# Optimization experiments

Measured on AMD Instinct MI355X. Metric: run time of the kernel, lower is better.

The kernel has to match this reference:

```python
import jax, jax.numpy as jnp
import numpy as np

N, E = 50000, 800000
IN_DIM, HID, HEADS, OUT_DIM = 7, 64, 4, 32
EPS = 1e-5


def gat_layer(x, src, dst, W, a_s, a_d, b, heads, ch, concat):
    # x: [N, F_in]; W: [F_in, heads*ch]; a_s,a_d: [heads, ch]; b: [heads*ch] or [ch]
    n = x.shape[0]
    h = (x @ W).reshape(n, heads, ch)
    e_src = jnp.sum(h * a_s, axis=-1)  # [N, heads]
    e_dst = jnp.sum(h * a_d, axis=-1)
    e = jax.nn.leaky_relu(e_src[src] + e_dst[dst], 0.2)  # [E, heads]
    m = jax.ops.segment_max(e, dst, num_segments=n)
    ex = jnp.exp(e - m[dst])
    denom = jax.ops.segment_sum(ex, dst, num_segments=n)
    alpha = ex / (denom[dst] + 1e-16)  # [E, heads]
    msg = h[src] * alpha[:, :, None]  # [E, heads, ch]
    out = jax.ops.segment_sum(msg, dst, num_segments=n)  # [N, heads, ch]
    out = out.reshape(n, heads * ch) if concat else out.mean(axis=1)
    return out + b


def batch_norm(x, g, be):
    mu = x.mean(axis=0)
    var = x.var(axis=0)
    return (x - mu) * jax.lax.rsqrt(var + EPS) * g + be


def setup_inputs() -> dict:
    key = jax.random.key(0)
    ks = jax.random.split(key, 24)
    d = {}
    d['x'] = jax.random.normal(ks[0], (N, IN_DIM), dtype=jnp.float32)
    d['edge_index'] = jax.random.randint(ks[1], (2, E), 0, N, dtype=jnp.int32)
    d['source_node'] = 123
    s = 0.1
    HC = HEADS * HID  # 256
    d['W1'] = jax.random.normal(ks[2], (IN_DIM, HC)) * s
    d['as1'] = jax.random.normal(ks[3], (HEADS, HID)) * s
    d['ad1'] = jax.random.normal(ks[4], (HEADS, HID)) * s
    d['b1'] = jnp.zeros((HC,))
    d['g1'] = jnp.ones((HC,))
    d['be1'] = jnp.zeros((HC,))
    d['W2'] = jax.random.normal(ks[5], (HC, HC)) * s
    d['as2'] = jax.random.normal(ks[6], (HEADS, HID)) * s
    d['ad2'] = jax.random.normal(ks[7], (HEADS, HID)) * s
    d['b2'] = jnp.zeros((HC,))
    d['g2'] = jnp.ones((HC,))
    d['be2'] = jnp.zeros((HC,))
    d['W3'] = jax.random.normal(ks[8], (HC, OUT_DIM)) * s
    d['as3'] = jax.random.normal(ks[9], (1, OUT_DIM)) * s
    d['ad3'] = jax.random.normal(ks[10], (1, OUT_DIM)) * s
    d['b3'] = jnp.zeros((OUT_DIM,))
    d['Wm1'] = jax.random.normal(ks[11], (2 * OUT_DIM, 64)) * s
    d['bm1'] = jnp.zeros((64,))
    d['Wm2'] = jax.random.normal(ks[12], (64, 32)) * s
    d['bm2'] = jnp.zeros((32,))
    d['Wm3'] = jax.random.normal(ks[13], (32, 1)) * s
    d['bm3'] = jnp.zeros((1,))
    return d


def reference(x, edge_index, source_node, W1, as1, ad1, b1, g1, be1,
              W2, as2, ad2, b2, g2, be2, W3, as3, ad3, b3,
              Wm1, bm1, Wm2, bm2, Wm3, bm3):
    n = x.shape[0]
    loop = jnp.arange(n, dtype=edge_index.dtype)
    src = jnp.concatenate([edge_index[0], loop])  # PyG GATConv adds self-loops
    dst = jnp.concatenate([edge_index[1], loop])
    h = gat_layer(x, src, dst, W1, as1, ad1, b1, HEADS, HID, True)
    h = jax.nn.relu(batch_norm(h, g1, be1))
    h = gat_layer(h, src, dst, W2, as2, ad2, b2, HEADS, HID, True)
    h = jax.nn.relu(batch_norm(h, g2, be2))
    emb = gat_layer(h, src, dst, W3, as3, ad3, b3, 1, OUT_DIM, False)  # [N, 32]
    src_emb = jnp.broadcast_to(emb[source_node][None, :], (n, OUT_DIM))
    z = jnp.concatenate([src_emb, emb], axis=1)  # [N, 64]
    z = jax.nn.relu(z @ Wm1 + bm1)
    z = jax.nn.relu(z @ Wm2 + bm2)
    scores = jax.nn.sigmoid(z @ Wm3 + bm3)
    return scores.squeeze(-1)
```

## Files before the change

kernel.cpp:

```cpp
#include <hip/hip_runtime.h>
#include <hip/hip_fp16.h>
#include <math.h>

#define NN 50000
#define EE 800000
#define ETOT (EE + NN)
#define HC 256
#define HEADS 4
#define OUTD 32
#define NB1 196

typedef _Float16 f16x8 __attribute__((ext_vector_type(8)));
typedef float f32x4 __attribute__((ext_vector_type(4)));

__device__ __forceinline__ float wred_sum(float v) {
#pragma unroll
  for (int off = 32; off; off >>= 1) v += __shfl_xor(v, off);
  return v;
}
__device__ __forceinline__ float lrelu(float x) { return x >= 0.f ? x : 0.2f * x; }

__global__ void zero_i32(int* __restrict__ p, int n) {
  int i = blockIdx.x * blockDim.x + threadIdx.x;
  if (i < n) p[i] = 0;
}

__global__ void hist_k(const int* __restrict__ ei, int* __restrict__ cnt) {
  int e = blockIdx.x * blockDim.x + threadIdx.x;
  if (e >= ETOT) return;
  int d = (e < EE) ? ei[EE + e] : (e - EE);
  atomicAdd(&cnt[d], 1);
}

__global__ void scan1_k(const int* __restrict__ cnt, int* __restrict__ part,
                        int* __restrict__ bsum) {
  __shared__ int s[256];
  int t = threadIdx.x, i = blockIdx.x * 256 + t;
  int v = (i < NN) ? cnt[i] : 0;
  s[t] = v;
  __syncthreads();
#pragma unroll
  for (int off = 1; off < 256; off <<= 1) {
    int u = (t >= off) ? s[t - off] : 0;
    __syncthreads();
    s[t] += u;
    __syncthreads();
  }
  if (i < NN) part[i] = s[t] - v;
  if (t == 255) bsum[blockIdx.x] = s[255];
}

__global__ void scan2_k(const int* __restrict__ bsum, int* __restrict__ bscan) {
  __shared__ int s[256];
  int t = threadIdx.x;
  int v = (t < NB1) ? bsum[t] : 0;
  s[t] = v;
  __syncthreads();
#pragma unroll
  for (int off = 1; off < 256; off <<= 1) {
    int u = (t >= off) ? s[t - off] : 0;
    __syncthreads();
    s[t] += u;
    __syncthreads();
  }
  if (t < NB1) bscan[t] = s[t] - v;
}

__global__ void scan3_k(const int* __restrict__ part, const int* __restrict__ bscan,
                        int* __restrict__ offs, int* __restrict__ cursor) {
  int i = blockIdx.x * 256 + threadIdx.x;
  if (i < NN) {
    int v = part[i] + bscan[blockIdx.x];
    offs[i] = v;
    cursor[i] = v;
  }
  if (i == 0) offs[NN] = ETOT;
}

__global__ void scatter_k(const int* __restrict__ ei, int* __restrict__ cursor,
                          int* __restrict__ elist) {
  int e = blockIdx.x * blockDim.x + threadIdx.x;
  if (e >= ETOT) return;
  int s, d;
  if (e < EE) { s = ei[e]; d = ei[EE + e]; } else { s = d = e - EE; }
  int pos = atomicAdd(&cursor[d], 1);
  elist[pos] = s;
}

template <int NCOL>
__global__ __launch_bounds__(256) void wswz_k(const float* __restrict__ W,
                                              __half* __restrict__ Bh) {
  int idx = blockIdx.x * 256 + threadIdx.x;
  if (idx >= HC * NCOL) return;
  int k = idx / NCOL, n = idx % NCOL;
  int frag = (n >> 4) * 8 + (k >> 5);
  int lane = (n & 15) + (((k >> 3) & 3) << 4);
  int elem = k & 7;
  Bh[(frag * 64 + lane) * 8 + elem] = __float2half(W[idx]);
}

__global__ __launch_bounds__(256) void l1_h_k(
    const float* __restrict__ x, const float* __restrict__ W1,
    const float* __restrict__ asf, const float* __restrict__ adf,
    __half* __restrict__ hb, float* __restrict__ es, float* __restrict__ ed) {
  int t = threadIdx.x, w = t >> 6;
  float wc[7];
#pragma unroll
  for (int k = 0; k < 7; ++k) wc[k] = W1[k * HC + t];
  float av = asf[t], dv = adf[t];
  for (int i = blockIdx.x; i < NN; i += gridDim.x) {
    float acc = 0.f;
#pragma unroll
    for (int k = 0; k < 7; ++k) acc = fmaf(x[i * 7 + k], wc[k], acc);
    hb[(size_t)i * HC + t] = __float2half(acc);
    float a = wred_sum(acc * av);
    float d = wred_sum(acc * dv);
    if ((t & 63) == 0) { es[i * HEADS + w] = a; ed[i * HEADS + w] = d; }
  }
}

__global__ __launch_bounds__(256) void gat_agg256(
    const __half* __restrict__ hb, const float* __restrict__ es,
    const float* __restrict__ ed, const int* __restrict__ offs,
    const int* __restrict__ elist, const float* __restrict__ bias,
    float* __restrict__ out) {
  int t = threadIdx.x, wv = t >> 6, lane = t & 63;
  int hd = lane >> 4;
  float4 bv = ((const float4*)bias)[lane];
  const float2* hb4 = (const float2*)hb;
  int i = blockIdx.x * 4 + wv;
  if (i >= NN) return;
  int base = offs[i], end = offs[i + 1];
  float edv = ed[i * HEADS + hd];
  float denom = 0.f;
  float4 acc = make_float4(0.f, 0.f, 0.f, 0.f);

#define EDGE1(SRC)                                         \
  {                                                        \
    int src_ = (SRC);                                      \
    float ex_ = __expf(lrelu(es[src_ * HEADS + hd] + edv));\
    denom += ex_;                                          \
    float2 raw_ = hb4[(size_t)src_ * 64 + lane];           \
    float2 h01_ = __half22float2(*(__half2*)&raw_.x);      \
    float2 h23_ = __half22float2(*(__half2*)&raw_.y);      \
    acc.x = fmaf(ex_, h01_.x, acc.x);                      \
    acc.y = fmaf(ex_, h01_.y, acc.y);                      \
    acc.z = fmaf(ex_, h23_.x, acc.z);                      \
    acc.w = fmaf(ex_, h23_.y, acc.w);                      \
  }

  int e = base;
  int alim = (base + 3) & ~3;
  for (; e < end && e < alim; ++e) EDGE1(elist[e]);
  for (; e + 4 <= end; e += 4) {
    int4 idx = *(const int4*)&elist[e];
    float e0 = es[idx.x * HEADS + hd], e1 = es[idx.y * HEADS + hd];
    float e2 = es[idx.z * HEADS + hd], e3 = es[idx.w * HEADS + hd];
    float2 r0 = hb4[(size_t)idx.x * 64 + lane];
    float2 r1 = hb4[(size_t)idx.y * 64 + lane];
    float2 r2 = hb4[(size_t)idx.z * 64 + lane];
    float2 r3 = hb4[(size_t)idx.w * 64 + lane];
    float x0 = __expf(lrelu(e0 + edv)), x1 = __expf(lrelu(e1 + edv));
    float x2 = __expf(lrelu(e2 + edv)), x3 = __expf(lrelu(e3 + edv));
    denom += (x0 + x1) + (x2 + x3);
    float2 a0 = __half22float2(*(__half2*)&r0.x), b0 = __half22float2(*(__half2*)&r0.y);
    float2 a1 = __half22float2(*(__half2*)&r1.x), b1 = __half22float2(*(__half2*)&r1.y);
    float2 a2 = __half22float2(*(__half2*)&r2.x), b2 = __half22float2(*(__half2*)&r2.y);
    float2 a3 = __half22float2(*(__half2*)&r3.x), b3 = __half22float2(*(__half2*)&r3.y);
    acc.x = fmaf(x0, a0.x, fmaf(x1, a1.x, fmaf(x2, a2.x, fmaf(x3, a3.x, acc.x))));
    acc.y = fmaf(x0, a0.y, fmaf(x1, a1.y, fmaf(x2, a2.y, fmaf(x3, a3.y, acc.y))));
    acc.z = fmaf(x0, b0.x, fmaf(x1, b1.x, fmaf(x2, b2.x, fmaf(x3, b3.x, acc.z))));
    acc.w = fmaf(x0, b0.y, fmaf(x1, b1.y, fmaf(x2, b2.y, fmaf(x3, b3.y, acc.w))));
  }
  for (; e < end; ++e) EDGE1(elist[e]);
#undef EDGE1

  float inv = 1.f / (denom + 1e-16f);
  float4 r;
  r.x = fmaf(acc.x, inv, bv.x);
  r.y = fmaf(acc.y, inv, bv.y);
  r.z = fmaf(acc.z, inv, bv.z);
  r.w = fmaf(acc.w, inv, bv.w);
  ((float4*)(out + (size_t)i * HC))[lane] = r;
}

__global__ __launch_bounds__(256) void bn_stats_k(const float* __restrict__ X,
                                                  float* __restrict__ sums) {
  int t = threadIdx.x;
  int r0 = blockIdx.x * 64;
  int rend = min(r0 + 64, NN);
  float s = 0.f, q = 0.f;
  for (int r = r0; r < rend; ++r) {
    float v = X[(size_t)r * HC + t];
    s += v;
    q = fmaf(v, v, q);
  }
  atomicAdd(&sums[t], s);
  atomicAdd(&sums[HC + t], q);
}

__global__ void bn_final_k(const float* __restrict__ sums, const float* __restrict__ g,
                           const float* __restrict__ be, float* __restrict__ ab) {
  int t = threadIdx.x;
  float mu = sums[t] * (1.f / NN);
  float var = sums[HC + t] * (1.f / NN) - mu * mu;
  float a = g[t] * rsqrtf(var + 1e-5f);
  ab[t] = a;
  ab[HC + t] = fmaf(-mu, a, be[t]);
}

__global__ __launch_bounds__(256) void gemm_mfma_k(const float* __restrict__ A,
                                                   const __half* __restrict__ Bh,
                                                   const float* __restrict__ ab,
                                                   __half* __restrict__ Ch) {
  __shared__ __align__(16) __half As[128 * 40];
  __shared__ float abL[512];
  int t = threadIdx.x;
  abL[t] = ab[t];
  abL[256 + t] = ab[256 + t];
  int wv = t >> 6, lane = t & 63;
  int wm = wv >> 1, wn = wv & 1;
  int m0 = blockIdx.x * 128;
  int ntb = blockIdx.y * 8 + wn * 4;
  int srow = t >> 1;
  int skq = (t & 1) * 16;
  int grow = m0 + srow;
  const f16x8* Bf = (const f16x8*)Bh;

  f32x4 acc[4][4];
  f32x4 zf = {0.f, 0.f, 0.f, 0.f};
#pragma unroll
  for (int mt = 0; mt < 4; ++mt)
#pragma unroll
    for (int nt = 0; nt < 4; ++nt) acc[mt][nt] = zf;

  for (int ks = 0; ks < 8; ++ks) {
    int k0 = ks * 32;
    __syncthreads();
    {
      float xv[16];
      if (grow < NN) {
        const float* ap = A + (size_t)grow * HC + k0 + skq;
#pragma unroll
        for (int q = 0; q < 4; ++q) *(float4*)&xv[q * 4] = *(const float4*)(ap + q * 4);
      } else {
#pragma unroll
        for (int j = 0; j < 16; ++j) xv[j] = 0.f;
      }
      f16x8 v0, v1;
#pragma unroll
      for (int j = 0; j < 8; ++j) {
        float a_ = abL[k0 + skq + j], b_ = abL[256 + k0 + skq + j];
        v0[j] = (_Float16)fmaxf(fmaf(xv[j], a_, b_), 0.f);
      }
#pragma unroll
      for (int j = 0; j < 8; ++j) {
        float a_ = abL[k0 + skq + 8 + j], b_ = abL[256 + k0 + skq + 8 + j];
        v1[j] = (_Float16)fmaxf(fmaf(xv[8 + j], a_, b_), 0.f);
      }
      *(f16x8*)&As[srow * 40 + skq] = v0;
      *(f16x8*)&As[srow * 40 + skq + 8] = v1;
    }
    __syncthreads();
    f16x8 af[4], bf[4];
    int lr = wm * 64 + (lane & 15);
    int kk = (lane >> 4) * 8;
#pragma unroll
    for (int mt = 0; mt < 4; ++mt)
      af[mt] = *(const f16x8*)&As[(lr + mt * 16) * 40 + kk];
#pragma unroll
    for (int nt = 0; nt < 4; ++nt)
      bf[nt] = Bf[(size_t)((ntb + nt) * 8 + ks) * 64 + lane];
#pragma unroll
    for (int mt = 0; mt < 4; ++mt)
#pragma unroll
      for (int nt = 0; nt < 4; ++nt)
        acc[mt][nt] = __builtin_amdgcn_mfma_f32_16x16x32_f16(af[mt], bf[nt], acc[mt][nt], 0, 0, 0);
  }

  int colb = blockIdx.y * 128 + wn * 64 + (lane & 15);
#pragma unroll
  for (int mt = 0; mt < 4; ++mt) {
    int rowb = m0 + wm * 64 + mt * 16 + (lane >> 4) * 4;
#pragma unroll
    for (int nt = 0; nt < 4; ++nt) {
      int col = colb + nt * 16;
#pragma unroll
      for (int r = 0; r < 4; ++r) {
        int row = rowb + r;
        if (row < NN) Ch[(size_t)row * HC + col] = __float2half(acc[mt][nt][r]);
      }
    }
  }
}

__global__ __launch_bounds__(256) void l3_mfma_k(const float* __restrict__ A,
                                                 const __half* __restrict__ Bh,
                                                 const float* __restrict__ ab,
                                                 float* __restrict__ h3) {
  __shared__ __align__(16) __half As[128 * 40];
  __shared__ float abL[512];
  int t = threadIdx.x;
  abL[t] = ab[t];
  abL[256 + t] = ab[256 + t];
  int wv = t >> 6, lane = t & 63;
  int m0 = blockIdx.x * 128;
  int srow = t >> 1;
  int skq = (t & 1) * 16;
  int grow = m0 + srow;
  const f16x8* Bf = (const f16x8*)Bh;

  f32x4 acc[2][2];
  f32x4 zf = {0.f, 0.f, 0.f, 0.f};
#pragma unroll
  for (int mt = 0; mt < 2; ++mt)
#pragma unroll
    for (int nt = 0; nt < 2; ++nt) acc[mt][nt] = zf;

  for (int ks = 0; ks < 8; ++ks) {
    int k0 = ks * 32;
    __syncthreads();
    {
      float xv[16];
      if (grow < NN) {
        const float* ap = A + (size_t)grow * HC + k0 + skq;
#pragma unroll
        for (int q = 0; q < 4; ++q) *(float4*)&xv[q * 4] = *(const float4*)(ap + q * 4);
      } else {
#pragma unroll
        for (int j = 0; j < 16; ++j) xv[j] = 0.f;
      }
      f16x8 v0, v1;
#pragma unroll
      for (int j = 0; j < 8; ++j) {
        float a_ = abL[k0 + skq + j], b_ = abL[256 + k0 + skq + j];
        v0[j] = (_Float16)fmaxf(fmaf(xv[j], a_, b_), 0.f);
      }
#pragma unroll
      for (int j = 0; j < 8; ++j) {
        float a_ = abL[k0 + skq + 8 + j], b_ = abL[256 + k0 + skq + 8 + j];
        v1[j] = (_Float16)fmaxf(fmaf(xv[8 + j], a_, b_), 0.f);
      }
      *(f16x8*)&As[srow * 40 + skq] = v0;
      *(f16x8*)&As[srow * 40 + skq + 8] = v1;
    }
    __syncthreads();
    f16x8 af[2], bf[2];
    int lr = wv * 32 + (lane & 15);
    int kk = (lane >> 4) * 8;
#pragma unroll
    for (int mt = 0; mt < 2; ++mt)
      af[mt] = *(const f16x8*)&As[(lr + mt * 16) * 40 + kk];
#pragma unroll
    for (int nt = 0; nt < 2; ++nt)
      bf[nt] = Bf[(size_t)(nt * 8 + ks) * 64 + lane];
#pragma unroll
    for (int mt = 0; mt < 2; ++mt)
#pragma unroll
      for (int nt = 0; nt < 2; ++nt)
        acc[mt][nt] = __builtin_amdgcn_mfma_f32_16x16x32_f16(af[mt], bf[nt], acc[mt][nt], 0, 0, 0);
  }

#pragma unroll
  for (int mt = 0; mt < 2; ++mt) {
    int rowb = m0 + wv * 32 + mt * 16 + (lane >> 4) * 4;
#pragma unroll
    for (int nt = 0; nt < 2; ++nt) {
      int col = nt * 16 + (lane & 15);
#pragma unroll
      for (int r = 0; r < 4; ++r) {
        int row = rowb + r;
        if (row < NN) h3[(size_t)row * OUTD + col] = acc[mt][nt][r];
      }
    }
  }
}

__global__ __launch_bounds__(256) void esed3_k(const float* __restrict__ h3,
                                               const float* __restrict__ asf,
                                               const float* __restrict__ adf,
                                               float* __restrict__ es3,
                                               float* __restrict__ ed3) {
  int t = threadIdx.x;
  int node = blockIdx.x * 8 + (t >> 5);
  int c = t & 31;
  if (node >= NN) return;
  float v = h3[(size_t)node * OUTD + c];
  float a = v * asf[c], d = v * adf[c];
#pragma unroll
  for (int off = 16; off; off >>= 1) {
    a += __shfl_xor(a, off);
    d += __shfl_xor(d, off);
  }
  if (c == 0) { es3[node] = a; ed3[node] = d; }
}

__global__ __launch_bounds__(256) void esed_k(const __half* __restrict__ hb,
                                              const float* __restrict__ asf,
                                              const float* __restrict__ adf,
                                              float* __restrict__ es,
                                              float* __restrict__ ed) {
  int t = threadIdx.x, w = t >> 6;
  float av = asf[t], dv = adf[t];
  for (int i = blockIdx.x; i < NN; i += gridDim.x) {
    float v = __half2float(hb[(size_t)i * HC + t]);
    float a = wred_sum(v * av);
    float d = wred_sum(v * dv);
    if ((t & 63) == 0) { es[i * HEADS + w] = a; ed[i * HEADS + w] = d; }
  }
}

__global__ __launch_bounds__(256) void gat_agg32(
    const float* __restrict__ h3, const float* __restrict__ es3,
    const float* __restrict__ ed3, const int* __restrict__ offs,
    const int* __restrict__ elist, const float* __restrict__ b3,
    float* __restrict__ emb) {
  int t = threadIdx.x, wv = t >> 6, lane = t & 63;
  int eo = lane >> 5, c = lane & 31;
  float bv = b3[c];
  int i = blockIdx.x * 4 + wv;
  if (i >= NN) return;
  int base = offs[i], end = offs[i + 1];
  float edv = ed3[i];
  float denom = 0.f, acc = 0.f;
#pragma unroll 2
  for (int e = base + eo; e < end; e += 2) {
    int src = elist[e];
    float ex = __expf(lrelu(es3[src] + edv));
    denom += ex;
    acc = fmaf(ex, h3[(size_t)src * OUTD + c], acc);
  }
  denom += __shfl_xor(denom, 32);
  acc += __shfl_xor(acc, 32);
  if (eo == 0) emb[(size_t)i * OUTD + c] = acc / (denom + 1e-16f) + bv;
}

__global__ void c1_k(const float* __restrict__ emb, const int* __restrict__ srcn,
                     const float* __restrict__ Wm1, const float* __restrict__ bm1,
                     float* __restrict__ c1) {
  int l = threadIdx.x;
  int sn = srcn[0];
  float a = bm1[l];
  for (int k = 0; k < 32; ++k) a = fmaf(emb[(size_t)sn * OUTD + k], Wm1[k * 64 + l], a);
  c1[l] = a;
}

__global__ __launch_bounds__(256) void mlp_k(
    const float* __restrict__ emb, const float* __restrict__ c1,
    const float* __restrict__ Wm1, const float* __restrict__ Wm2,
    const float* __restrict__ bm2, const float* __restrict__ Wm3,
    const float* __restrict__ bm3, float* __restrict__ outp) {
  __shared__ float WL1s[32][64];
  __shared__ float WL2s[64][32];
  __shared__ float W3s[32];
  __shared__ float c1s[64];
  int t = threadIdx.x;
  for (int q = t; q < 2048; q += 256) WL1s[q >> 6][q & 63] = Wm1[(32 + (q >> 6)) * 64 + (q & 63)];
  for (int q = t; q < 2048; q += 256) WL2s[q >> 5][q & 31] = Wm2[q];
  if (t < 32) W3s[t] = Wm3[t];
  if (t < 64) c1s[t] = c1[t];
  __syncthreads();
  int wv = t >> 6, lane = t & 63;
  int p = lane >> 5, c = lane & 31;
  float bm2v = bm2[c];
  float bm3v = bm3[0];
  for (int node = blockIdx.x * 4 + wv; node < NN; node += gridDim.x * 4) {
    float zv = (lane < 32) ? emb[(size_t)node * OUTD + lane] : 0.f;
    float a1 = c1s[lane];
#pragma unroll
    for (int k = 0; k < 32; ++k) a1 = fmaf(__shfl(zv, k), WL1s[k][lane], a1);
    float u1 = fmaxf(a1, 0.f);
    float a2 = 0.f;
#pragma unroll
    for (int j = 0; j < 32; ++j) a2 = fmaf(__shfl(u1, p * 32 + j), WL2s[p * 32 + j][c], a2);
    a2 += __shfl_xor(a2, 32);
    float v = 0.f;
    if (lane < 32) {
      float u2 = fmaxf(a2 + bm2v, 0.f);
      v = u2 * W3s[c];
    }
    v = wred_sum(v);
    if (lane == 0) outp[node] = 1.f / (1.f + __expf(-(v + bm3v)));
  }
}

extern "C" void kernel_launch(void* const* d_in, const int* in_sizes, int n_in,
                              void* d_out, int out_size, void* d_ws, size_t ws_size,
                              hipStream_t stream) {
  const float* x   = (const float*)d_in[0];
  const int* eidx  = (const int*)d_in[1];
  const int* srcn  = (const int*)d_in[2];
  const float* W1  = (const float*)d_in[3];
  const float* as1 = (const float*)d_in[4];
  const float* ad1 = (const float*)d_in[5];
  const float* b1  = (const float*)d_in[6];
  const float* g1  = (const float*)d_in[7];
  const float* be1 = (const float*)d_in[8];
  const float* W2  = (const float*)d_in[9];
  const float* as2 = (const float*)d_in[10];
  const float* ad2 = (const float*)d_in[11];
  const float* b2  = (const float*)d_in[12];
  const float* g2  = (const float*)d_in[13];
  const float* be2 = (const float*)d_in[14];
  const float* W3  = (const float*)d_in[15];
  const float* as3 = (const float*)d_in[16];
  const float* ad3 = (const float*)d_in[17];
  const float* b3  = (const float*)d_in[18];
  const float* Wm1 = (const float*)d_in[19];
  const float* bm1 = (const float*)d_in[20];
  const float* Wm2 = (const float*)d_in[21];
  const float* bm2 = (const float*)d_in[22];
  const float* Wm3 = (const float*)d_in[23];
  const float* bm3 = (const float*)d_in[24];
  float* outp = (float*)d_out;

  float* fw = (float*)d_ws;
  float* bufB   = fw;  fw += (size_t)NN * HC;
  __half* hbuf  = (__half*)fw; fw += (size_t)NN * HC / 2;
  float* h3     = fw;  fw += (size_t)NN * OUTD;
  float* emb    = fw;  fw += (size_t)NN * OUTD;
  float* es     = fw;  fw += (size_t)NN * HEADS;
  float* ed     = fw;  fw += (size_t)NN * HEADS;
  float* es3    = fw;  fw += NN;
  float* ed3    = fw;  fw += NN;
  float* bnsums = fw;  fw += 2 * HC;
  float* bnab   = fw;  fw += 2 * HC;
  float* c1     = fw;  fw += 64;
  __half* Bh    = (__half*)fw; fw += (size_t)HC * HC / 2;
  __half* Bh3   = (__half*)fw; fw += (size_t)HC * OUTD / 2;
  int* iw = (int*)fw;
  int* offs   = iw;  iw += NN + 4;
  int* cursor = iw;  iw += NN;
  int* elist  = iw;  iw += ETOT;
  int* part   = iw;  iw += NN;
  int* bsum   = iw;  iw += 256;
  int* bscan  = iw;  iw += 256;

  const int TB = 256;
  const int gE = (ETOT + TB - 1) / TB;
  const int gN4 = (NN + 3) / 4;

  zero_i32<<<(NN + TB - 1) / TB, TB, 0, stream>>>(cursor, NN);
  hist_k<<<gE, TB, 0, stream>>>(eidx, cursor);
  scan1_k<<<NB1, TB, 0, stream>>>(cursor, part, bsum);
  scan2_k<<<1, TB, 0, stream>>>(bsum, bscan);
  scan3_k<<<NB1, TB, 0, stream>>>(part, bscan, offs, cursor);
  scatter_k<<<gE, TB, 0, stream>>>(eidx, cursor, elist);
  wswz_k<HC><<<HC * HC / TB, TB, 0, stream>>>(W2, Bh);
  wswz_k<OUTD><<<HC * OUTD / TB, TB, 0, stream>>>(W3, Bh3);

  l1_h_k<<<2048, TB, 0, stream>>>(x, W1, as1, ad1, hbuf, es, ed);
  gat_agg256<<<gN4, TB, 0, stream>>>(hbuf, es, ed, offs, elist, b1, bufB);
  zero_i32<<<2, TB, 0, stream>>>((int*)bnsums, 2 * HC);
  bn_stats_k<<<(NN + 63) / 64, TB, 0, stream>>>(bufB, bnsums);
  bn_final_k<<<1, TB, 0, stream>>>(bnsums, g1, be1, bnab);

  gemm_mfma_k<<<dim3((NN + 127) / 128, HC / 128), TB, 0, stream>>>(bufB, Bh, bnab, hbuf);
  esed_k<<<2048, TB, 0, stream>>>(hbuf, as2, ad2, es, ed);
  gat_agg256<<<gN4, TB, 0, stream>>>(hbuf, es, ed, offs, elist, b2, bufB);
  zero_i32<<<2, TB, 0, stream>>>((int*)bnsums, 2 * HC);
  bn_stats_k<<<(NN + 63) / 64, TB, 0, stream>>>(bufB, bnsums);
  bn_final_k<<<1, TB, 0, stream>>>(bnsums, g2, be2, bnab);

  l3_mfma_k<<<(NN + 127) / 128, TB, 0, stream>>>(bufB, Bh3, bnab, h3);
  esed3_k<<<(NN + 7) / 8, TB, 0, stream>>>(h3, as3, ad3, es3, ed3);
  gat_agg32<<<gN4, TB, 0, stream>>>(h3, es3, ed3, offs, elist, b3, emb);

  c1_k<<<1, 64, 0, stream>>>(emb, srcn, Wm1, bm1, c1);
  mlp_k<<<512, TB, 0, stream>>>(emb, c1, Wm1, Wm2, bm2, Wm3, bm3, outp);
}
```

Baseline: 514.0 us.

## Store aggregation outputs in fp16 and fuse attention scores into GEMM epilogues

```diff
diff --git a/kernel.cpp b/kernel.cpp
--- a/kernel.cpp
+++ b/kernel.cpp
@@ -16,6 +16,11 @@
 __device__ __forceinline__ float wred_sum(float v) {
 #pragma unroll
   for (int off = 32; off; off >>= 1) v += __shfl_xor(v, off);
+  return v;
+}
+__device__ __forceinline__ float qred16(float v) {
+#pragma unroll
+  for (int off = 1; off < 16; off <<= 1) v += __shfl_xor(v, off);
   return v;
 }
 __device__ __forceinline__ float lrelu(float x) { return x >= 0.f ? x : 0.2f * x; }
@@ -123,7 +128,7 @@
     const __half* __restrict__ hb, const float* __restrict__ es,
     const float* __restrict__ ed, const int* __restrict__ offs,
     const int* __restrict__ elist, const float* __restrict__ bias,
-    float* __restrict__ out) {
+    __half* __restrict__ out) {
   int t = threadIdx.x, wv = t >> 6, lane = t & 63;
   int hd = lane >> 4;
   float4 bv = ((const float4*)bias)[lane];
@@ -135,63 +140,84 @@
   float denom = 0.f;
   float4 acc = make_float4(0.f, 0.f, 0.f, 0.f);
 
-#define EDGE1(SRC)                                         \
-  {                                                        \
-    int src_ = (SRC);                                      \
-    float ex_ = __expf(lrelu(es[src_ * HEADS + hd] + edv));\
-    denom += ex_;                                          \
-    float2 raw_ = hb4[(size_t)src_ * 64 + lane];           \
-    float2 h01_ = __half22float2(*(__half2*)&raw_.x);      \
-    float2 h23_ = __half22float2(*(__half2*)&raw_.y);      \
-    acc.x = fmaf(ex_, h01_.x, acc.x);                      \
-    acc.y = fmaf(ex_, h01_.y, acc.y);                      \
-    acc.z = fmaf(ex_, h23_.x, acc.z);                      \
-    acc.w = fmaf(ex_, h23_.y, acc.w);                      \
+#define ACC1(X_, R_)                                   \
+  {                                                    \
+    float2 h01_ = __half22float2(*(__half2*)&R_.x);    \
+    float2 h23_ = __half22float2(*(__half2*)&R_.y);    \
+    acc.x = fmaf(X_, h01_.x, acc.x);                   \
+    acc.y = fmaf(X_, h01_.y, acc.y);                   \
+    acc.z = fmaf(X_, h23_.x, acc.z);                   \
+    acc.w = fmaf(X_, h23_.y, acc.w);                   \
+  }
+#define EDGE1(SRC)                                          \
+  {                                                         \
+    int src_ = (SRC);                                       \
+    float ex_ = __expf(lrelu(es[src_ * HEADS + hd] + edv)); \
+    denom += ex_;                                           \
+    float2 raw_ = hb4[(size_t)src_ * 64 + lane];            \
+    ACC1(ex_, raw_);                                        \
   }
 
   int e = base;
   int alim = (base + 3) & ~3;
   for (; e < end && e < alim; ++e) EDGE1(elist[e]);
+  for (; e + 8 <= end; e += 8) {
+    int4 ia = *(const int4*)&elist[e];
+    int4 ib = *(const int4*)&elist[e + 4];
+    float f0 = es[ia.x * HEADS + hd], f1 = es[ia.y * HEADS + hd];
+    float f2 = es[ia.z * HEADS + hd], f3 = es[ia.w * HEADS + hd];
+    float f4 = es[ib.x * HEADS + hd], f5 = es[ib.y * HEADS + hd];
+    float f6 = es[ib.z * HEADS + hd], f7 = es[ib.w * HEADS + hd];
+    float2 r0 = hb4[(size_t)ia.x * 64 + lane];
+    float2 r1 = hb4[(size_t)ia.y * 64 + lane];
+    float2 r2 = hb4[(size_t)ia.z * 64 + lane];
+    float2 r3 = hb4[(size_t)ia.w * 64 + lane];
+    float2 r4 = hb4[(size_t)ib.x * 64 + lane];
+    float2 r5 = hb4[(size_t)ib.y * 64 + lane];
+    float2 r6 = hb4[(size_t)ib.z * 64 + lane];
+    float2 r7 = hb4[(size_t)ib.w * 64 + lane];
+    float x0 = __expf(lrelu(f0 + edv)), x1 = __expf(lrelu(f1 + edv));
+    float x2 = __expf(lrelu(f2 + edv)), x3 = __expf(lrelu(f3 + edv));
+    float x4 = __expf(lrelu(f4 + edv)), x5 = __expf(lrelu(f5 + edv));
+    float x6 = __expf(lrelu(f6 + edv)), x7 = __expf(lrelu(f7 + edv));
+    denom += ((x0 + x1) + (x2 + x3)) + ((x4 + x5) + (x6 + x7));
+    ACC1(x0, r0); ACC1(x1, r1); ACC1(x2, r2); ACC1(x3, r3);
+    ACC1(x4, r4); ACC1(x5, r5); ACC1(x6, r6); ACC1(x7, r7);
+  }
   for (; e + 4 <= end; e += 4) {
-    int4 idx = *(const int4*)&elist[e];
-    float e0 = es[idx.x * HEADS + hd], e1 = es[idx.y * HEADS + hd];
-    float e2 = es[idx.z * HEADS + hd], e3 = es[idx.w * HEADS + hd];
-    float2 r0 = hb4[(size_t)idx.x * 64 + lane];
-    float2 r1 = hb4[(size_t)idx.y * 64 + lane];
-    float2 r2 = hb4[(size_t)idx.z * 64 + lane];
-    float2 r3 = hb4[(size_t)idx.w * 64 + lane];
-    float x0 = __expf(lrelu(e0 + edv)), x1 = __expf(lrelu(e1 + edv));
-    float x2 = __expf(lrelu(e2 + edv)), x3 = __expf(lrelu(e3 + edv));
+    int4 ia = *(const int4*)&elist[e];
+    float f0 = es[ia.x * HEADS + hd], f1 = es[ia.y * HEADS + hd];
+    float f2 = es[ia.z * HEADS + hd], f3 = es[ia.w * HEADS + hd];
+    float2 r0 = hb4[(size_t)ia.x * 64 + lane];
+    float2 r1 = hb4[(size_t)ia.y * 64 + lane];
+    float2 r2 = hb4[(size_t)ia.z * 64 + lane];
+    float2 r3 = hb4[(size_t)ia.w * 64 + lane];
+    float x0 = __expf(lrelu(f0 + edv)), x1 = __expf(lrelu(f1 + edv));
+    float x2 = __expf(lrelu(f2 + edv)), x3 = __expf(lrelu(f3 + edv));
     denom += (x0 + x1) + (x2 + x3);
-    float2 a0 = __half22float2(*(__half2*)&r0.x), b0 = __half22float2(*(__half2*)&r0.y);
-    float2 a1 = __half22float2(*(__half2*)&r1.x), b1 = __half22float2(*(__half2*)&r1.y);
-    float2 a2 = __half22float2(*(__half2*)&r2.x), b2 = __half22float2(*(__half2*)&r2.y);
-    float2 a3 = __half22float2(*(__half2*)&r3.x), b3 = __half22float2(*(__half2*)&r3.y);
-    acc.x = fmaf(x0, a0.x, fmaf(x1, a1.x, fmaf(x2, a2.x, fmaf(x3, a3.x, acc.x))));
-    acc.y = fmaf(x0, a0.y, fmaf(x1, a1.y, fmaf(x2, a2.y, fmaf(x3, a3.y, acc.y))));
-    acc.z = fmaf(x0, b0.x, fmaf(x1, b1.x, fmaf(x2, b2.x, fmaf(x3, b3.x, acc.z))));
-    acc.w = fmaf(x0, b0.y, fmaf(x1, b1.y, fmaf(x2, b2.y, fmaf(x3, b3.y, acc.w))));
+    ACC1(x0, r0); ACC1(x1, r1); ACC1(x2, r2); ACC1(x3, r3);
   }
   for (; e < end; ++e) EDGE1(elist[e]);
 #undef EDGE1
+#undef ACC1
 
   float inv = 1.f / (denom + 1e-16f);
-  float4 r;
-  r.x = fmaf(acc.x, inv, bv.x);
-  r.y = fmaf(acc.y, inv, bv.y);
-  r.z = fmaf(acc.z, inv, bv.z);
-  r.w = fmaf(acc.w, inv, bv.w);
-  ((float4*)(out + (size_t)i * HC))[lane] = r;
-}
-
-__global__ __launch_bounds__(256) void bn_stats_k(const float* __restrict__ X,
+  __half2 o01 = __floats2half2_rn(fmaf(acc.x, inv, bv.x), fmaf(acc.y, inv, bv.y));
+  __half2 o23 = __floats2half2_rn(fmaf(acc.z, inv, bv.z), fmaf(acc.w, inv, bv.w));
+  uint2 pk;
+  pk.x = *(unsigned int*)&o01;
+  pk.y = *(unsigned int*)&o23;
+  ((uint2*)(out + (size_t)i * HC))[lane] = pk;
+}
+
+__global__ __launch_bounds__(256) void bn_stats_k(const __half* __restrict__ X,
                                                   float* __restrict__ sums) {
   int t = threadIdx.x;
   int r0 = blockIdx.x * 64;
   int rend = min(r0 + 64, NN);
   float s = 0.f, q = 0.f;
   for (int r = r0; r < rend; ++r) {
-    float v = X[(size_t)r * HC + t];
+    float v = __half2float(X[(size_t)r * HC + t]);
     s += v;
     q = fmaf(v, v, q);
   }
@@ -209,10 +235,14 @@
   ab[HC + t] = fmaf(-mu, a, be[t]);
 }
 
-__global__ __launch_bounds__(256) void gemm_mfma_k(const float* __restrict__ A,
+__global__ __launch_bounds__(256) void gemm_mfma_k(const __half* __restrict__ A,
                                                    const __half* __restrict__ Bh,
                                                    const float* __restrict__ ab,
-                                                   __half* __restrict__ Ch) {
+                                                   const float* __restrict__ asf,
+                                                   const float* __restrict__ adf,
+                                                   __half* __restrict__ Ch,
+                                                   float* __restrict__ es,
+                                                   float* __restrict__ ed) {
   __shared__ __align__(16) __half As[128 * 40];
   __shared__ float abL[512];
   int t = threadIdx.x;
@@ -240,9 +270,16 @@
     {
       float xv[16];
       if (grow < NN) {
-        const float* ap = A + (size_t)grow * HC + k0 + skq;
-#pragma unroll
-        for (int q = 0; q < 4; ++q) *(float4*)&xv[q * 4] = *(const float4*)(ap + q * 4);
+        const __half* ap = A + (size_t)grow * HC + k0 + skq;
+        __half2 hp[8];
+        *(uint4*)&hp[0] = *(const uint4*)ap;
+        *(uint4*)&hp[4] = *(const uint4*)(ap + 8);
+#pragma unroll
+        for (int j = 0; j < 8; ++j) {
+          float2 f = __half22float2(hp[j]);
+          xv[2 * j] = f.x;
+          xv[2 * j + 1] = f.y;
+        }
       } else {
 #pragma unroll
         for (int j = 0; j < 16; ++j) xv[j] = 0.f;
@@ -292,12 +329,43 @@
       }
     }
   }
-}
-
-__global__ __launch_bounds__(256) void l3_mfma_k(const float* __restrict__ A,
+  float asv[4], adv[4];
+#pragma unroll
+  for (int nt = 0; nt < 4; ++nt) {
+    asv[nt] = asf[colb + nt * 16];
+    adv[nt] = adf[colb + nt * 16];
+  }
+  int head = (blockIdx.y << 1) | wn;
+#pragma unroll
+  for (int mt = 0; mt < 4; ++mt) {
+    int rowb = m0 + wm * 64 + mt * 16 + (lane >> 4) * 4;
+#pragma unroll
+    for (int r = 0; r < 4; ++r) {
+      float pe = 0.f, pd = 0.f;
+#pragma unroll
+      for (int nt = 0; nt < 4; ++nt) {
+        pe = fmaf(acc[mt][nt][r], asv[nt], pe);
+        pd = fmaf(acc[mt][nt][r], adv[nt], pd);
+      }
+      pe = qred16(pe);
+      pd = qred16(pd);
+      int row = rowb + r;
+      if ((lane & 15) == 0 && row < NN) {
+        es[row * HEADS + head] = pe;
+        ed[row * HEADS + head] = pd;
+      }
+    }
+  }
+}
+
+__global__ __launch_bounds__(256) void l3_mfma_k(const __half* __restrict__ A,
                                                  const __half* __restrict__ Bh,
                                                  const float* __restrict__ ab,
-                                                 float* __restrict__ h3) {
+                                                 const float* __restrict__ asf,
+                                                 const float* __restrict__ adf,
+                                                 __half* __restrict__ h3,
+                                                 float* __restrict__ es3,
+                                                 float* __restrict__ ed3) {
   __shared__ __align__(16) __half As[128 * 40];
   __shared__ float abL[512];
   int t = threadIdx.x;
@@ -323,9 +391,16 @@
     {
       float xv[16];
       if (grow < NN) {
-        const float* ap = A + (size_t)grow * HC + k0 + skq;
-#pragma unroll
-        for (int q = 0; q < 4; ++q) *(float4*)&xv[q * 4] = *(const float4*)(ap + q * 4);
+        const __half* ap = A + (size_t)grow * HC + k0 + skq;
+        __half2 hp[8];
+        *(uint4*)&hp[0] = *(const uint4*)ap;
+        *(uint4*)&hp[4] = *(const uint4*)(ap + 8);
+#pragma unroll
+        for (int j = 0; j < 8; ++j) {
+          float2 f = __half22float2(hp[j]);
+          xv[2 * j] = f.x;
+          xv[2 * j + 1] = f.y;
+        }
       } else {
 #pragma unroll
         for (int j = 0; j < 16; ++j) xv[j] = 0.f;
@@ -361,57 +436,38 @@
         acc[mt][nt] = __builtin_amdgcn_mfma_f32_16x16x32_f16(af[mt], bf[nt], acc[mt][nt], 0, 0, 0);
   }
 
+  float as3v[2], ad3v[2];
+#pragma unroll
+  for (int nt = 0; nt < 2; ++nt) {
+    as3v[nt] = asf[nt * 16 + (lane & 15)];
+    ad3v[nt] = adf[nt * 16 + (lane & 15)];
+  }
 #pragma unroll
   for (int mt = 0; mt < 2; ++mt) {
     int rowb = m0 + wv * 32 + mt * 16 + (lane >> 4) * 4;
 #pragma unroll
-    for (int nt = 0; nt < 2; ++nt) {
-      int col = nt * 16 + (lane & 15);
-#pragma unroll
-      for (int r = 0; r < 4; ++r) {
-        int row = rowb + r;
-        if (row < NN) h3[(size_t)row * OUTD + col] = acc[mt][nt][r];
+    for (int r = 0; r < 4; ++r) {
+      int row = rowb + r;
+      float pe = 0.f, pd = 0.f;
+#pragma unroll
+      for (int nt = 0; nt < 2; ++nt) {
+        int col = nt * 16 + (lane & 15);
+        if (row < NN) h3[(size_t)row * OUTD + col] = __float2half(acc[mt][nt][r]);
+        pe = fmaf(acc[mt][nt][r], as3v[nt], pe);
+        pd = fmaf(acc[mt][nt][r], ad3v[nt], pd);
+      }
+      pe = qred16(pe);
+      pd = qred16(pd);
+      if ((lane & 15) == 0 && row < NN) {
+        es3[row] = pe;
+        ed3[row] = pd;
       }
     }
   }
 }
 
-__global__ __launch_bounds__(256) void esed3_k(const float* __restrict__ h3,
-                                               const float* __restrict__ asf,
-                                               const float* __restrict__ adf,
-                                               float* __restrict__ es3,
-                                               float* __restrict__ ed3) {
-  int t = threadIdx.x;
-  int node = blockIdx.x * 8 + (t >> 5);
-  int c = t & 31;
-  if (node >= NN) return;
-  float v = h3[(size_t)node * OUTD + c];
-  float a = v * asf[c], d = v * adf[c];
-#pragma unroll
-  for (int off = 16; off; off >>= 1) {
-    a += __shfl_xor(a, off);
-    d += __shfl_xor(d, off);
-  }
-  if (c == 0) { es3[node] = a; ed3[node] = d; }
-}
-
-__global__ __launch_bounds__(256) void esed_k(const __half* __restrict__ hb,
-                                              const float* __restrict__ asf,
-                                              const float* __restrict__ adf,
-                                              float* __restrict__ es,
-                                              float* __restrict__ ed) {
-  int t = threadIdx.x, w = t >> 6;
-  float av = asf[t], dv = adf[t];
-  for (int i = blockIdx.x; i < NN; i += gridDim.x) {
-    float v = __half2float(hb[(size_t)i * HC + t]);
-    float a = wred_sum(v * av);
-    float d = wred_sum(v * dv);
-    if ((t & 63) == 0) { es[i * HEADS + w] = a; ed[i * HEADS + w] = d; }
-  }
-}
-
 __global__ __launch_bounds__(256) void gat_agg32(
-    const float* __restrict__ h3, const float* __restrict__ es3,
+    const __half* __restrict__ h3, const float* __restrict__ es3,
     const float* __restrict__ ed3, const int* __restrict__ offs,
     const int* __restrict__ elist, const float* __restrict__ b3,
     float* __restrict__ emb) {
@@ -428,7 +484,7 @@
     int src = elist[e];
     float ex = __expf(lrelu(es3[src] + edv));
     denom += ex;
-    acc = fmaf(ex, h3[(size_t)src * OUTD + c], acc);
+    acc = fmaf(ex, __half2float(h3[(size_t)src * OUTD + c]), acc);
   }
   denom += __shfl_xor(denom, 32);
   acc += __shfl_xor(acc, 32);
@@ -514,27 +570,31 @@
   const float* bm3 = (const float*)d_in[24];
   float* outp = (float*)d_out;
 
-  float* fw = (float*)d_ws;
-  float* bufB   = fw;  fw += (size_t)NN * HC;
-  __half* hbuf  = (__half*)fw; fw += (size_t)NN * HC / 2;
-  float* h3     = fw;  fw += (size_t)NN * OUTD;
-  float* emb    = fw;  fw += (size_t)NN * OUTD;
-  float* es     = fw;  fw += (size_t)NN * HEADS;
-  float* ed     = fw;  fw += (size_t)NN * HEADS;
-  float* es3    = fw;  fw += NN;
-  float* ed3    = fw;  fw += NN;
-  float* bnsums = fw;  fw += 2 * HC;
-  float* bnab   = fw;  fw += 2 * HC;
-  float* c1     = fw;  fw += 64;
-  __half* Bh    = (__half*)fw; fw += (size_t)HC * HC / 2;
-  __half* Bh3   = (__half*)fw; fw += (size_t)HC * OUTD / 2;
-  int* iw = (int*)fw;
-  int* offs   = iw;  iw += NN + 4;
-  int* cursor = iw;  iw += NN;
-  int* elist  = iw;  iw += ETOT;
-  int* part   = iw;  iw += NN;
-  int* bsum   = iw;  iw += 256;
-  int* bscan  = iw;  iw += 256;
+  char* wp = (char*)d_ws;
+  auto carve = [&](size_t bytes) {
+    void* p = (void*)wp;
+    wp += (bytes + 255) & ~(size_t)255;
+    return p;
+  };
+  __half* aggB  = (__half*)carve((size_t)NN * HC * 2);
+  __half* hbuf  = (__half*)carve((size_t)NN * HC * 2);
+  __half* h3h   = (__half*)carve((size_t)NN * OUTD * 2);
+  float* emb    = (float*)carve((size_t)NN * OUTD * 4);
+  float* es     = (float*)carve((size_t)NN * HEADS * 4);
+  float* ed     = (float*)carve((size_t)NN * HEADS * 4);
+  float* es3    = (float*)carve((size_t)NN * 4);
+  float* ed3    = (float*)carve((size_t)NN * 4);
+  float* bnsums = (float*)carve(2 * HC * 4);
+  float* bnab   = (float*)carve(2 * HC * 4);
+  float* c1     = (float*)carve(64 * 4);
+  __half* Bh    = (__half*)carve((size_t)HC * HC * 2);
+  __half* Bh3   = (__half*)carve((size_t)HC * OUTD * 2);
+  int* offs     = (int*)carve((NN + 4) * 4);
+  int* cursor   = (int*)carve(NN * 4);
+  int* elist    = (int*)carve((size_t)ETOT * 4);
+  int* part     = (int*)carve(NN * 4);
+  int* bsum     = (int*)carve(256 * 4);
+  int* bscan    = (int*)carve(256 * 4);
 
   const int TB = 256;
   const int gE = (ETOT + TB - 1) / TB;
@@ -550,21 +610,20 @@
   wswz_k<OUTD><<<HC * OUTD / TB, TB, 0, stream>>>(W3, Bh3);
 
   l1_h_k<<<2048, TB, 0, stream>>>(x, W1, as1, ad1, hbuf, es, ed);
-  gat_agg256<<<gN4, TB, 0, stream>>>(hbuf, es, ed, offs, elist, b1, bufB);
+  gat_agg256<<<gN4, TB, 0, stream>>>(hbuf, es, ed, offs, elist, b1, aggB);
   zero_i32<<<2, TB, 0, stream>>>((int*)bnsums, 2 * HC);
-  bn_stats_k<<<(NN + 63) / 64, TB, 0, stream>>>(bufB, bnsums);
+  bn_stats_k<<<(NN + 63) / 64, TB, 0, stream>>>(aggB, bnsums);
   bn_final_k<<<1, TB, 0, stream>>>(bnsums, g1, be1, bnab);
 
-  gemm_mfma_k<<<dim3((NN + 127) / 128, HC / 128), TB, 0, stream>>>(bufB, Bh, bnab, hbuf);
-  esed_k<<<2048, TB, 0, stream>>>(hbuf, as2, ad2, es, ed);
-  gat_agg256<<<gN4, TB, 0, stream>>>(hbuf, es, ed, offs, elist, b2, bufB);
+  gemm_mfma_k<<<dim3((NN + 127) / 128, HC / 128), TB, 0, stream>>>(aggB, Bh, bnab, as2, ad2,
+                                                                   hbuf, es, ed);
+  gat_agg256<<<gN4, TB, 0, stream>>>(hbuf, es, ed, offs, elist, b2, aggB);
   zero_i32<<<2, TB, 0, stream>>>((int*)bnsums, 2 * HC);
-  bn_stats_k<<<(NN + 63) / 64, TB, 0, stream>>>(bufB, bnsums);
+  bn_stats_k<<<(NN + 63) / 64, TB, 0, stream>>>(aggB, bnsums);
   bn_final_k<<<1, TB, 0, stream>>>(bnsums, g2, be2, bnab);
 
-  l3_mfma_k<<<(NN + 127) / 128, TB, 0, stream>>>(bufB, Bh3, bnab, h3);
-  esed3_k<<<(NN + 7) / 8, TB, 0, stream>>>(h3, as3, ad3, es3, ed3);
-  gat_agg32<<<gN4, TB, 0, stream>>>(h3, es3, ed3, offs, elist, b3, emb);
+  l3_mfma_k<<<(NN + 127) / 128, TB, 0, stream>>>(aggB, Bh3, bnab, as3, ad3, h3h, es3, ed3);
+  gat_agg32<<<gN4, TB, 0, stream>>>(h3h, es3, ed3, offs, elist, b3, emb);
 
   c1_k<<<1, 64, 0, stream>>>(emb, srcn, Wm1, bm1, c1);
   mlp_k<<<512, TB, 0, stream>>>(emb, c1, Wm1, Wm2, bm2, Wm3, bm3, outp);
```

After: 464.0 us. 9.7% less time.
